# Kernel tuning notes

Hardware: AMD Instinct MI355X
Metric: run time of the kernel (lower is better)

## Reference

```python
import jax, jax.numpy as jnp
import numpy as np

B, H, S, D = 4, 16, 2048, 64


def setup_inputs() -> dict:
    key = jax.random.key(0)
    kq, kk, kv = jax.random.split(key, 3)
    q = jax.random.normal(kq, (B, H, S, D), dtype=jnp.float32)
    k = jax.random.normal(kk, (B, H, S, D), dtype=jnp.float32)
    v = jax.random.normal(kv, (B, H, S, D), dtype=jnp.float32)
    # causal mask: 1 = keep, 0 = masked (matches masked_fill(mask == 0, -10000))
    mask = jnp.tril(jnp.ones((S, S), dtype=jnp.int32))[None, None, :, :]
    return {"q": q, "k": k, "v": v, "mask": mask}


def reference(q, k, v, mask):
    head_dim = q.shape[3]
    # [b,h,s,t] attention logits
    attn = jnp.einsum("bhsd,bhtd->bhst", q, k) / jnp.sqrt(jnp.float32(head_dim))
    attn = jnp.where(mask == 0, jnp.float32(-10000.0), attn)
    score = jax.nn.softmax(attn, axis=-1)
    # dropout is identity at inference (eval mode)
    return jnp.einsum("bhst,bhtd->bhsd", score, v)
```

## Files before the change

kernel.cpp:

```cpp
#include <hip/hip_runtime.h>
#include <hip/hip_bf16.h>

typedef __bf16 bf16_t;
typedef bf16_t bf16x8 __attribute__((ext_vector_type(8)));
typedef bf16_t bf16x4 __attribute__((ext_vector_type(4)));
typedef float  f32x4  __attribute__((ext_vector_type(4)));

#define KT 64
#define DH 64


__global__ __launch_bounds__(512, 4)
void sdpa_fwd(const float* __restrict__ Qg, const float* __restrict__ Kg,
              const float* __restrict__ Vg, float* __restrict__ Og)
{
    __shared__ bf16_t kbuf[KT * DH];
    __shared__ bf16_t vbuf[DH * KT];
    __shared__ bf16_t pbuf[8 * 16 * KT];

    const int n  = blockIdx.x;
    const int o  = ((n & 7) << 6) | (n >> 3);
    const int bh = o >> 3;
    const int pr = o & 7;

    const int t   = threadIdx.x;
    const int w   = t >> 6;
    const int l15 = t & 15;
    const int lg  = (t >> 4) & 3;

    const size_t hoff = (size_t)bh * 2048 * DH;
    const float* Qh = Qg + hoff;
    const float* Kh = Kg + hoff;
    const float* Vh = Vg + hoff;
    float*       Oh = Og + hoff;

    const int skey = t >> 3;
    const int sdc  = t & 7;

    f32x4 pk0, pk1, pv0, pv1;

    const int stripes[2] = { 15 - pr, pr };
    const int ntile[2]   = { 2*(15-pr) + 2, 2*pr + 2 };

    {
        const float* kp = Kh + (size_t)skey * DH + sdc * 8;
        pk0 = *(const f32x4*)kp;  pk1 = *(const f32x4*)(kp + 4);
        const float* vp = Vh + (size_t)skey * DH + sdc * 8;
        pv0 = *(const f32x4*)vp;  pv1 = *(const f32x4*)(vp + 4);
    }

    for (int s = 0; s < 2; ++s) {
        const int qS   = stripes[s] * 128;
        const int nkt  = ntile[s];
        const int qsb  = qS + w * 16;
        const int qrow = qsb + l15;

        bf16x8 qf[2];
        {
            const float* qp = Qh + (size_t)qrow * DH + lg * 8;
#pragma unroll
            for (int dh2 = 0; dh2 < 2; ++dh2) {
                f32x4 a = *(const f32x4*)(qp + dh2 * 32);
                f32x4 b = *(const f32x4*)(qp + dh2 * 32 + 4);
                bf16x8 f;
                f[0] = (bf16_t)(a[0]*0.125f); f[1] = (bf16_t)(a[1]*0.125f);
                f[2] = (bf16_t)(a[2]*0.125f); f[3] = (bf16_t)(a[3]*0.125f);
                f[4] = (bf16_t)(b[0]*0.125f); f[5] = (bf16_t)(b[1]*0.125f);
                f[6] = (bf16_t)(b[2]*0.125f); f[7] = (bf16_t)(b[3]*0.125f);
                qf[dh2] = f;
            }
        }

        f32x4 acc[4];
#pragma unroll
        for (int ng = 0; ng < 4; ++ng) { f32x4 z = {0.f,0.f,0.f,0.f}; acc[ng] = z; }
        float m_run = -1e30f, l_run = 0.0f;

        for (int kt = 0; kt < nkt; ++kt) {
            __syncthreads();
            {
                bf16x8 f;
                f[0] = (bf16_t)pk0[0]; f[1] = (bf16_t)pk0[1];
                f[2] = (bf16_t)pk0[2]; f[3] = (bf16_t)pk0[3];
                f[4] = (bf16_t)pk1[0]; f[5] = (bf16_t)pk1[1];
                f[6] = (bf16_t)pk1[2]; f[7] = (bf16_t)pk1[3];
                *(bf16x8*)((char*)kbuf + skey*128 + ((sdc ^ (skey & 7)) << 4)) = f;
                float vv[8] = { pv0[0],pv0[1],pv0[2],pv0[3], pv1[0],pv1[1],pv1[2],pv1[3] };
#pragma unroll
                for (int j = 0; j < 8; ++j) {
                    const int byte = (sdc*8 + j)*128
                                   + ((((skey >> 3) ^ j ^ sdc) & 7) << 4)
                                   + (skey & 7) * 2;
                    *(bf16_t*)((char*)vbuf + byte) = (bf16_t)vv[j];
                }
            }
            const bool last = (s == 1) && (kt == nkt - 1);
            if (!last) {
                const int nk = (kt + 1 < nkt) ? kt + 1 : 0;
                const float* kp = Kh + (size_t)(nk*KT + skey) * DH + sdc * 8;
                pk0 = *(const f32x4*)kp;  pk1 = *(const f32x4*)(kp + 4);
                const float* vp = Vh + (size_t)(nk*KT + skey) * DH + sdc * 8;
                pv0 = *(const f32x4*)vp;  pv1 = *(const f32x4*)(vp + 4);
            }
            __syncthreads();

            if (kt * KT > qsb + 15) continue;

            f32x4 tf[4];
#pragma unroll
            for (int kg = 0; kg < 4; ++kg) {
                f32x4 c = {0.f,0.f,0.f,0.f};
#pragma unroll
                for (int dh2 = 0; dh2 < 2; ++dh2) {
                    const int byte = (kg*16 + l15)*128 + (((dh2*4 + lg) ^ (l15 & 7)) << 4);
                    const bf16x8 kf = *(const bf16x8*)((const char*)kbuf + byte);
                    c = __builtin_amdgcn_mfma_f32_16x16x32_bf16(kf, qf[dh2], c, 0, 0, 0);
                }
                tf[kg] = c;
            }

            const bool need_mask = (kt*KT + KT - 1) > qsb;
            float mx = -1e30f;
#pragma unroll
            for (int kg = 0; kg < 4; ++kg) {
#pragma unroll
                for (int r = 0; r < 4; ++r) {
                    float sv = tf[kg][r];
                    if (need_mask) {
                        const int key = kt*KT + kg*16 + lg*4 + r;
                        if (key > qrow) sv = -10000.0f;
                    }
                    tf[kg][r] = sv;
                    mx = fmaxf(mx, sv);
                }
            }
            mx = fmaxf(mx, __shfl_xor(mx, 16));
            mx = fmaxf(mx, __shfl_xor(mx, 32));
            const float mnew  = fmaxf(m_run, mx);
            const float alpha = __expf(m_run - mnew);
            m_run = mnew;

            float sum = 0.0f;
#pragma unroll
            for (int kg = 0; kg < 4; ++kg) {
#pragma unroll
                for (int r = 0; r < 4; ++r) {
                    const float p = __expf(tf[kg][r] - mnew);
                    tf[kg][r] = p;
                    sum += p;
                }
            }
            sum += __shfl_xor(sum, 16);
            sum += __shfl_xor(sum, 32);
            l_run = l_run * alpha + sum;
#pragma unroll
            for (int ng = 0; ng < 4; ++ng) acc[ng] *= alpha;

            bf16_t* pq = pbuf + w * (16 * KT);
            const int prow = l15 * 128;
            const int pswz = l15 & 7;
#pragma unroll
            for (int kg = 0; kg < 4; ++kg) {
                bf16x4 t4;
                t4[0] = (bf16_t)tf[kg][0]; t4[1] = (bf16_t)tf[kg][1];
                t4[2] = (bf16_t)tf[kg][2]; t4[3] = (bf16_t)tf[kg][3];
                const int byte = prow + (((kg*2 + (lg >> 1)) ^ pswz) << 4) + (lg & 1)*8;
                *(bf16x4*)((char*)pq + byte) = t4;
            }
            asm volatile("s_waitcnt lgkmcnt(0)" ::: "memory");
            __builtin_amdgcn_sched_barrier(0);

#pragma unroll
            for (int kfi = 0; kfi < 2; ++kfi) {
                const int pbyte = prow + (((kfi*4 + lg) ^ pswz) << 4);
                const bf16x8 pf = *(const bf16x8*)((const char*)pq + pbyte);
#pragma unroll
                for (int ng = 0; ng < 4; ++ng) {
                    const int vbyte = (ng*16 + l15)*128
                        + ((((kfi*4 + lg) ^ (l15 & 7) ^ ((ng*2 + (l15 >> 3)) & 7)) ) << 4);
                    const bf16x8 vf = *(const bf16x8*)((const char*)vbuf + vbyte);
                    acc[ng] = __builtin_amdgcn_mfma_f32_16x16x32_bf16(vf, pf, acc[ng], 0, 0, 0);
                }
            }
        }

        const float inv = 1.0f / l_run;
        float* op = Oh + (size_t)qrow * DH + lg * 4;
#pragma unroll
        for (int ng = 0; ng < 4; ++ng) {
            f32x4 v = acc[ng];
            v *= inv;
            *(f32x4*)(op + ng * 16) = v;
        }
    }
}

extern "C" void kernel_launch(void* const* d_in, const int* in_sizes, int n_in,
                              void* d_out, int out_size, void* d_ws, size_t ws_size,
                              hipStream_t stream) {
    (void)in_sizes; (void)n_in; (void)d_ws; (void)ws_size; (void)out_size;
    const float* q = (const float*)d_in[0];
    const float* k = (const float*)d_in[1];
    const float* v = (const float*)d_in[2];
    float* out = (float*)d_out;
    hipLaunchKernelGGL(sdpa_fwd, dim3(512), dim3(512), 0, stream, q, k, v, out);
}
```

Before: 84.74 us.

## Switch to 32x32 MFMA with register-resident P and double-buffered K/V tiles

Replaces the 16x16x32 MFMA tiling with 32x32x16 MFMAs so each wave handles 32 query rows. The softmax probabilities are passed from the QK result to the PV operand through a permlane32 swap in registers instead of going through LDS, which removes the per-wave P buffer and its wait. K/V tiles are double-buffered in LDS so only one barrier per tile is needed. The work split also changes from paired 128-row stripes to one 256-row stripe per block in reverse order, and output rescaling is skipped when the running max grows by less than 8. That lazy rescale trades exactness of the running max for fewer exp and multiply operations, and the single-stripe split may leave blocks with uneven work.

Measured after the change: 132.5 us. 56.3% more time.

```diff
diff --git a/kernel.cpp b/kernel.cpp
--- a/kernel.cpp
+++ b/kernel.cpp
@@ -3,30 +3,36 @@
 
 typedef __bf16 bf16_t;
 typedef bf16_t bf16x8 __attribute__((ext_vector_type(8)));
-typedef bf16_t bf16x4 __attribute__((ext_vector_type(4)));
 typedef float  f32x4  __attribute__((ext_vector_type(4)));
-
-#define KT 64
+typedef float  f32x16 __attribute__((ext_vector_type(16)));
+typedef int    i32x4  __attribute__((ext_vector_type(4)));
+
 #define DH 64
+
+__device__ __forceinline__ unsigned pkbf(float a, float b) {
+    union { bf16_t h[2]; unsigned u; } z;
+    z.h[0] = (bf16_t)a; z.h[1] = (bf16_t)b;
+    return z.u;
+}
 
 
 __global__ __launch_bounds__(512, 4)
 void sdpa_fwd(const float* __restrict__ Qg, const float* __restrict__ Kg,
               const float* __restrict__ Vg, float* __restrict__ Og)
 {
-    __shared__ bf16_t kbuf[KT * DH];
-    __shared__ bf16_t vbuf[DH * KT];
-    __shared__ bf16_t pbuf[8 * 16 * KT];
-
-    const int n  = blockIdx.x;
-    const int o  = ((n & 7) << 6) | (n >> 3);
-    const int bh = o >> 3;
-    const int pr = o & 7;
+    __shared__ char lds[2 * 16384];
+
+    const int n   = blockIdx.x;
+    const int qi  = 7 - (n >> 6);
+    const int bh  = ((n & 7) << 3) | ((n >> 3) & 7);
+    const int qS  = qi * 256;
+    const int nkt = 4 * qi + 4;
 
     const int t   = threadIdx.x;
     const int w   = t >> 6;
-    const int l15 = t & 15;
-    const int lg  = (t >> 4) & 3;
+    const int l31 = t & 31;
+    const int hi  = (t >> 5) & 1;
+    const int swk = (l31 & 7) << 4;
 
     const size_t hoff = (size_t)bh * 2048 * DH;
     const float* Qh = Qg + hoff;
@@ -34,164 +40,161 @@
     const float* Vh = Vg + hoff;
     float*       Oh = Og + hoff;
 
+    const int qsb  = qS + w * 32;
+    const int qrow = qsb + l31;
+    const int ktd  = qsb >> 6;
+
+    bf16x8 qf[4];
+#pragma unroll
+    for (int sd = 0; sd < 4; ++sd) {
+        const float* qp = Qh + (size_t)qrow * DH + sd * 16 + hi * 8;
+        f32x4 a = *(const f32x4*)qp;
+        f32x4 b = *(const f32x4*)(qp + 4);
+        bf16x8 f;
+        f[0] = (bf16_t)(a[0]*0.125f); f[1] = (bf16_t)(a[1]*0.125f);
+        f[2] = (bf16_t)(a[2]*0.125f); f[3] = (bf16_t)(a[3]*0.125f);
+        f[4] = (bf16_t)(b[0]*0.125f); f[5] = (bf16_t)(b[1]*0.125f);
+        f[6] = (bf16_t)(b[2]*0.125f); f[7] = (bf16_t)(b[3]*0.125f);
+        qf[sd] = f;
+    }
+
+    f32x16 acc0 = {}, acc1 = {};
+    float m_run = -1e30f, l_run = 0.0f;
+
     const int skey = t >> 3;
     const int sdc  = t & 7;
 
-    f32x4 pk0, pk1, pv0, pv1;
-
-    const int stripes[2] = { 15 - pr, pr };
-    const int ntile[2]   = { 2*(15-pr) + 2, 2*pr + 2 };
-
+    f32x4 rk0, rk1, rv0, rv1;
     {
         const float* kp = Kh + (size_t)skey * DH + sdc * 8;
-        pk0 = *(const f32x4*)kp;  pk1 = *(const f32x4*)(kp + 4);
+        rk0 = *(const f32x4*)kp;  rk1 = *(const f32x4*)(kp + 4);
         const float* vp = Vh + (size_t)skey * DH + sdc * 8;
-        pv0 = *(const f32x4*)vp;  pv1 = *(const f32x4*)(vp + 4);
-    }
-
-    for (int s = 0; s < 2; ++s) {
-        const int qS   = stripes[s] * 128;
-        const int nkt  = ntile[s];
-        const int qsb  = qS + w * 16;
-        const int qrow = qsb + l15;
-
-        bf16x8 qf[2];
+        rv0 = *(const f32x4*)vp;  rv1 = *(const f32x4*)(vp + 4);
+    }
+
+    for (int kt = 0; kt < nkt; ++kt) {
+        char* kb_ = lds + (kt & 1) * 16384;
+        char* vb_ = kb_ + 8192;
+
         {
-            const float* qp = Qh + (size_t)qrow * DH + lg * 8;
-#pragma unroll
-            for (int dh2 = 0; dh2 < 2; ++dh2) {
-                f32x4 a = *(const f32x4*)(qp + dh2 * 32);
-                f32x4 b = *(const f32x4*)(qp + dh2 * 32 + 4);
-                bf16x8 f;
-                f[0] = (bf16_t)(a[0]*0.125f); f[1] = (bf16_t)(a[1]*0.125f);
-                f[2] = (bf16_t)(a[2]*0.125f); f[3] = (bf16_t)(a[3]*0.125f);
-                f[4] = (bf16_t)(b[0]*0.125f); f[5] = (bf16_t)(b[1]*0.125f);
-                f[6] = (bf16_t)(b[2]*0.125f); f[7] = (bf16_t)(b[3]*0.125f);
-                qf[dh2] = f;
+            bf16x8 f;
+            f[0] = (bf16_t)rk0[0]; f[1] = (bf16_t)rk0[1];
+            f[2] = (bf16_t)rk0[2]; f[3] = (bf16_t)rk0[3];
+            f[4] = (bf16_t)rk1[0]; f[5] = (bf16_t)rk1[1];
+            f[6] = (bf16_t)rk1[2]; f[7] = (bf16_t)rk1[3];
+            *(bf16x8*)(kb_ + ((skey * 128 + sdc * 16) ^ ((skey & 7) << 4))) = f;
+#pragma unroll
+            for (int jj = 0; jj < 8; ++jj) {
+                const float x = (jj < 4) ? rv0[jj & 3] : rv1[jj & 3];
+                const int d = sdc * 8 + jj;
+                *(bf16_t*)(vb_ + ((d * 128 + skey * 2) ^ ((jj ^ sdc) << 4))) = (bf16_t)x;
             }
         }
-
-        f32x4 acc[4];
-#pragma unroll
-        for (int ng = 0; ng < 4; ++ng) { f32x4 z = {0.f,0.f,0.f,0.f}; acc[ng] = z; }
-        float m_run = -1e30f, l_run = 0.0f;
-
-        for (int kt = 0; kt < nkt; ++kt) {
-            __syncthreads();
-            {
-                bf16x8 f;
-                f[0] = (bf16_t)pk0[0]; f[1] = (bf16_t)pk0[1];
-                f[2] = (bf16_t)pk0[2]; f[3] = (bf16_t)pk0[3];
-                f[4] = (bf16_t)pk1[0]; f[5] = (bf16_t)pk1[1];
-                f[6] = (bf16_t)pk1[2]; f[7] = (bf16_t)pk1[3];
-                *(bf16x8*)((char*)kbuf + skey*128 + ((sdc ^ (skey & 7)) << 4)) = f;
-                float vv[8] = { pv0[0],pv0[1],pv0[2],pv0[3], pv1[0],pv1[1],pv1[2],pv1[3] };
-#pragma unroll
-                for (int j = 0; j < 8; ++j) {
-                    const int byte = (sdc*8 + j)*128
-                                   + ((((skey >> 3) ^ j ^ sdc) & 7) << 4)
-                                   + (skey & 7) * 2;
-                    *(bf16_t*)((char*)vbuf + byte) = (bf16_t)vv[j];
+        if (kt + 1 < nkt) {
+            const float* kp = Kh + (size_t)((kt + 1) * 64 + skey) * DH + sdc * 8;
+            rk0 = *(const f32x4*)kp;  rk1 = *(const f32x4*)(kp + 4);
+            const float* vp = Vh + (size_t)((kt + 1) * 64 + skey) * DH + sdc * 8;
+            rv0 = *(const f32x4*)vp;  rv1 = *(const f32x4*)(vp + 4);
+        }
+        __syncthreads();
+
+        if (kt * 64 <= qsb + 31) {
+            f32x16 tf0 = {}, tf1 = {};
+#pragma unroll
+            for (int sd = 0; sd < 4; ++sd) {
+                const int inner = sd * 32 + hi * 16;
+                const bf16x8 k0 = *(const bf16x8*)(kb_ + ((l31 * 128 + inner) ^ swk));
+                const bf16x8 k1 = *(const bf16x8*)(kb_ + (((32 + l31) * 128 + inner) ^ swk));
+                tf0 = __builtin_amdgcn_mfma_f32_32x32x16_bf16(k0, qf[sd], tf0, 0, 0, 0);
+                tf1 = __builtin_amdgcn_mfma_f32_32x32x16_bf16(k1, qf[sd], tf1, 0, 0, 0);
+            }
+
+            if (kt == ktd) {
+#pragma unroll
+                for (int r = 0; r < 16; ++r) {
+                    const int krow = kt * 64 + (r & 3) + 8 * (r >> 2) + 4 * hi;
+                    if (krow > qrow)      tf0[r] = -10000.0f;
+                    if (krow + 32 > qrow) tf1[r] = -10000.0f;
                 }
             }
-            const bool last = (s == 1) && (kt == nkt - 1);
-            if (!last) {
-                const int nk = (kt + 1 < nkt) ? kt + 1 : 0;
-                const float* kp = Kh + (size_t)(nk*KT + skey) * DH + sdc * 8;
-                pk0 = *(const f32x4*)kp;  pk1 = *(const f32x4*)(kp + 4);
-                const float* vp = Vh + (size_t)(nk*KT + skey) * DH + sdc * 8;
-                pv0 = *(const f32x4*)vp;  pv1 = *(const f32x4*)(vp + 4);
-            }
-            __syncthreads();
-
-            if (kt * KT > qsb + 15) continue;
-
-            f32x4 tf[4];
-#pragma unroll
-            for (int kg = 0; kg < 4; ++kg) {
-                f32x4 c = {0.f,0.f,0.f,0.f};
-#pragma unroll
-                for (int dh2 = 0; dh2 < 2; ++dh2) {
-                    const int byte = (kg*16 + l15)*128 + (((dh2*4 + lg) ^ (l15 & 7)) << 4);
-                    const bf16x8 kf = *(const bf16x8*)((const char*)kbuf + byte);
-                    c = __builtin_amdgcn_mfma_f32_16x16x32_bf16(kf, qf[dh2], c, 0, 0, 0);
-                }
-                tf[kg] = c;
-            }
-
-            const bool need_mask = (kt*KT + KT - 1) > qsb;
-            float mx = -1e30f;
-#pragma unroll
-            for (int kg = 0; kg < 4; ++kg) {
-#pragma unroll
-                for (int r = 0; r < 4; ++r) {
-                    float sv = tf[kg][r];
-                    if (need_mask) {
-                        const int key = kt*KT + kg*16 + lg*4 + r;
-                        if (key > qrow) sv = -10000.0f;
-                    }
-                    tf[kg][r] = sv;
-                    mx = fmaxf(mx, sv);
-                }
-            }
-            mx = fmaxf(mx, __shfl_xor(mx, 16));
+
+            float mx = tf0[0];
+#pragma unroll
+            for (int r = 1; r < 16; ++r) mx = fmaxf(mx, tf0[r]);
+#pragma unroll
+            for (int r = 0; r < 16; ++r) mx = fmaxf(mx, tf1[r]);
             mx = fmaxf(mx, __shfl_xor(mx, 32));
-            const float mnew  = fmaxf(m_run, mx);
-            const float alpha = __expf(m_run - mnew);
-            m_run = mnew;
+
+            if (!__all(mx <= m_run + 8.0f)) {
+                const float mnew  = fmaxf(m_run, mx);
+                const float alpha = __expf(m_run - mnew);
+                m_run = mnew;
+                l_run *= alpha;
+                acc0 *= alpha;
+                acc1 *= alpha;
+            }
 
             float sum = 0.0f;
 #pragma unroll
-            for (int kg = 0; kg < 4; ++kg) {
-#pragma unroll
-                for (int r = 0; r < 4; ++r) {
-                    const float p = __expf(tf[kg][r] - mnew);
-                    tf[kg][r] = p;
-                    sum += p;
-                }
-            }
-            sum += __shfl_xor(sum, 16);
+            for (int r = 0; r < 16; ++r) { tf0[r] = __expf(tf0[r] - m_run); sum += tf0[r]; }
+#pragma unroll
+            for (int r = 0; r < 16; ++r) { tf1[r] = __expf(tf1[r] - m_run); sum += tf1[r]; }
             sum += __shfl_xor(sum, 32);
-            l_run = l_run * alpha + sum;
-#pragma unroll
-            for (int ng = 0; ng < 4; ++ng) acc[ng] *= alpha;
-
-            bf16_t* pq = pbuf + w * (16 * KT);
-            const int prow = l15 * 128;
-            const int pswz = l15 & 7;
-#pragma unroll
-            for (int kg = 0; kg < 4; ++kg) {
-                bf16x4 t4;
-                t4[0] = (bf16_t)tf[kg][0]; t4[1] = (bf16_t)tf[kg][1];
-                t4[2] = (bf16_t)tf[kg][2]; t4[3] = (bf16_t)tf[kg][3];
-                const int byte = prow + (((kg*2 + (lg >> 1)) ^ pswz) << 4) + (lg & 1)*8;
-                *(bf16x4*)((char*)pq + byte) = t4;
-            }
-            asm volatile("s_waitcnt lgkmcnt(0)" ::: "memory");
-            __builtin_amdgcn_sched_barrier(0);
-
-#pragma unroll
-            for (int kfi = 0; kfi < 2; ++kfi) {
-                const int pbyte = prow + (((kfi*4 + lg) ^ pswz) << 4);
-                const bf16x8 pf = *(const bf16x8*)((const char*)pq + pbyte);
-#pragma unroll
-                for (int ng = 0; ng < 4; ++ng) {
-                    const int vbyte = (ng*16 + l15)*128
-                        + ((((kfi*4 + lg) ^ (l15 & 7) ^ ((ng*2 + (l15 >> 3)) & 7)) ) << 4);
-                    const bf16x8 vf = *(const bf16x8*)((const char*)vbuf + vbyte);
-                    acc[ng] = __builtin_amdgcn_mfma_f32_16x16x32_bf16(vf, pf, acc[ng], 0, 0, 0);
-                }
+            l_run += sum;
+
+            unsigned P0[2][4], P1[2][4];
+#pragma unroll
+            for (int rg = 0; rg < 4; ++rg) {
+                P0[0][rg] = pkbf(tf0[rg * 4 + 0], tf0[rg * 4 + 1]);
+                P1[0][rg] = pkbf(tf0[rg * 4 + 2], tf0[rg * 4 + 3]);
+                P0[1][rg] = pkbf(tf1[rg * 4 + 0], tf1[rg * 4 + 1]);
+                P1[1][rg] = pkbf(tf1[rg * 4 + 2], tf1[rg * 4 + 3]);
+            }
+
+#pragma unroll
+            for (int s = 0; s < 4; ++s) {
+                const int kb  = s >> 1;
+                const int rgl = (s & 1) * 2, rgh = rgl + 1;
+                int w0, w1, w2, w3;
+#if defined(__has_builtin) && __has_builtin(__builtin_amdgcn_permlane32_swap)
+                auto r0 = __builtin_amdgcn_permlane32_swap((int)P0[kb][rgl], (int)P0[kb][rgh], false, false);
+                auto r1 = __builtin_amdgcn_permlane32_swap((int)P1[kb][rgl], (int)P1[kb][rgh], false, false);
+                w0 = r0[0]; w2 = r0[1]; w1 = r1[0]; w3 = r1[1];
+#else
+                const int sa0 = __shfl_xor((int)P0[kb][rgl], 32);
+                const int sb0 = __shfl_xor((int)P0[kb][rgh], 32);
+                const int sa1 = __shfl_xor((int)P1[kb][rgl], 32);
+                const int sb1 = __shfl_xor((int)P1[kb][rgh], 32);
+                w0 = hi ? sb0 : (int)P0[kb][rgl];
+                w2 = hi ? (int)P0[kb][rgh] : sa0;
+                w1 = hi ? sb1 : (int)P1[kb][rgl];
+                w3 = hi ? (int)P1[kb][rgh] : sa1;
+#endif
+                union { i32x4 i; bf16x8 v; } pz;
+                pz.i = (i32x4){ w0, w1, w2, w3 };
+
+                const int inner = s * 32 + hi * 16;
+                const int d0 = l31;
+                const int d1 = 32 + l31;
+                const int sz0 = ((d0 & 7) ^ (d0 >> 3)) << 4;
+                const int sz1 = ((d1 & 7) ^ (d1 >> 3)) << 4;
+                const bf16x8 v0 = *(const bf16x8*)(vb_ + ((d0 * 128 + inner) ^ sz0));
+                const bf16x8 v1 = *(const bf16x8*)(vb_ + ((d1 * 128 + inner) ^ sz1));
+                acc0 = __builtin_amdgcn_mfma_f32_32x32x16_bf16(v0, pz.v, acc0, 0, 0, 0);
+                acc1 = __builtin_amdgcn_mfma_f32_32x32x16_bf16(v1, pz.v, acc1, 0, 0, 0);
             }
         }
-
-        const float inv = 1.0f / l_run;
-        float* op = Oh + (size_t)qrow * DH + lg * 4;
-#pragma unroll
-        for (int ng = 0; ng < 4; ++ng) {
-            f32x4 v = acc[ng];
-            v *= inv;
-            *(f32x4*)(op + ng * 16) = v;
-        }
+    }
+
+    const float inv = 1.0f / l_run;
+    float* op = Oh + (size_t)qrow * DH;
+#pragma unroll
+    for (int rq = 0; rq < 4; ++rq) {
+        f32x4 o0, o1;
+#pragma unroll
+        for (int j = 0; j < 4; ++j) { o0[j] = acc0[rq * 4 + j] * inv; o1[j] = acc1[rq * 4 + j] * inv; }
+        *(f32x4*)(op + 8 * rq + 4 * hi)      = o0;
+        *(f32x4*)(op + 32 + 8 * rq + 4 * hi) = o1;
     }
 }
 
```
